# Performance work log

Measured on AMD Instinct MI355X. Metric: run time of the kernel, lower is better.

## Reference

```python
import jax, jax.numpy as jnp
import numpy as np

N = 100000      # nodes
E = 3200000     # edges (avg degree 32)
NIN = 16        # node_input_channels
ECH = 16        # edge_channels
F = 10          # node_feature_channels
OUT = 32        # output_channels
ITERS = 3


def _lin(k, fan_in, fan_out):
    kw, kb = jax.random.split(k)
    s = 1.0 / np.sqrt(fan_in)
    W = jax.random.uniform(kw, (fan_in, fan_out), jnp.float32, -s, s)
    b = jax.random.uniform(kb, (fan_out,), jnp.float32, -s, s)
    return W, b


def setup_inputs() -> dict:
    key = jax.random.key(0)
    ks = jax.random.split(key, 11)
    x = jax.random.normal(ks[0], (N, NIN), jnp.float32)
    edge_index = jax.random.randint(ks[1], (2, E), 0, N, jnp.int64)
    edge_attr = jax.random.normal(ks[2], (E, ECH), jnp.float32)
    W1, b1 = _lin(ks[3], NIN, F)
    W2, b2 = _lin(ks[4], F, F)
    W3, b3 = _lin(ks[5], F, F)
    W4, b4 = _lin(ks[6], ECH, F)
    W5, b5 = _lin(ks[7], 2 * F, OUT)
    W6, b6 = _lin(ks[8], F, F)
    W7, b7 = _lin(ks[9], F, F)
    return dict(x=x, edge_index=edge_index, edge_attr=edge_attr,
                W1=W1, b1=b1, W2=W2, b2=b2, W3=W3, b3=b3, W4=W4, b4=b4,
                W5=W5, b5=b5, W6=W6, b6=b6, W7=W7, b7=b7)


def reference(x, edge_index, edge_attr, W1, b1, W2, b2, W3, b3, W4, b4, W5, b5, W6, b6, W7, b7):
    src = edge_index[0]
    dst = edge_index[1]
    n = x.shape[0]

    # loop-invariant pieces (same math, hoisted)
    o1 = x @ W1 + b1                                   # lin1(x), [N, F]
    e = jax.nn.relu(edge_attr @ W4 + b4)               # relu(lin4(edge_attr)), [E, F]
    o3 = jax.ops.segment_sum(e, dst, num_segments=n) @ W3 + b3  # lin3(scatter_add)

    features = jnp.zeros((n, F), x.dtype)
    for _ in range(ITERS):
        # scatter_add over edges with self-loops == segment_sum + identity
        agg = jax.ops.segment_sum(features[src], dst, num_segments=n) + features
        o2 = agg @ W2 + b2
        features = jax.nn.relu(o1 + o2 + o3)

    g = features.sum(axis=0) @ W6 + b6                 # lin6(sum), [F]
    h1 = jnp.broadcast_to(g, (n, F))                   # repeat over nodes
    h2 = features @ W7 + b7                            # lin7(features)
    out = jax.nn.relu(jnp.concatenate([h1, h2], axis=1)) @ W5 + b5
    return out
```

## Files before the change

### kernel.cpp

```cpp
#include <hip/hip_runtime.h>

#define NN 100000
#define NE 3200000
#define NIN 16
#define ECH 16
#define F 10
#define FP 16
#define OC 32
#define CSB 104
#define BKSH 7
#define NBK 782
#define CH 8192
#define CAP 5120

__device__ __forceinline__ unsigned pk_bf16(float a, float b) {
    unsigned ua = __float_as_uint(a); ua = (ua + 0x7FFFu + ((ua >> 16) & 1u)) >> 16;
    unsigned ub = __float_as_uint(b); ub = (ub + 0x7FFFu + ((ub >> 16) & 1u)) >> 16;
    return ua | (ub << 16);
}
__device__ __forceinline__ float bf_lo(unsigned u) { return __uint_as_float(u << 16); }
__device__ __forceinline__ float bf_hi(unsigned u) { return __uint_as_float(u & 0xFFFF0000u); }

__global__ __launch_bounds__(256) void k_binscat(
    const int* __restrict__ src, const int* __restrict__ dst,
    int* __restrict__ cur, int2* __restrict__ pair)
{
    __shared__ int lcnt[NBK];
    __shared__ int lbb[NBK];
    int t = threadIdx.x;
    int e0 = blockIdx.x * CH;
    int e1 = e0 + CH; if (e1 > NE) e1 = NE;
    for (int k = t; k < NBK; k += 256) lcnt[k] = 0;
    __syncthreads();
    for (int e = e0 + t; e < e1; e += 256)
        atomicAdd(&lcnt[dst[e] >> BKSH], 1);
    __syncthreads();
    for (int k = t; k < NBK; k += 256) {
        int c = lcnt[k];
        lbb[k] = c ? (k * CAP + atomicAdd(&cur[k], c)) : 0;
        lcnt[k] = 0;
    }
    __syncthreads();
    for (int e = e0 + t; e < e1; e += 256) {
        int d = dst[e];
        int bk = d >> BKSH;
        int idx = atomicAdd(&lcnt[bk], 1);
        pair[lbb[bk] + idx] = make_int2(src[e], ((d & 127) << 22) | e);
    }
}

__global__ __launch_bounds__(1024) void k_bkscan(const int* __restrict__ cnt,
                                                 int* __restrict__ bkbase,
                                                 int* __restrict__ offs)
{
    __shared__ int wsum[16], wscan[16];
    int t = threadIdx.x;
    int v = (t < NBK) ? cnt[t] : 0;
    int lane = t & 63, w = t >> 6;
    int inc = v;
    for (int d = 1; d < 64; d <<= 1) { int u = __shfl_up(inc, d); if (lane >= d) inc += u; }
    if (lane == 63) wsum[w] = inc;
    __syncthreads();
    if (t < 16) {
        int u = wsum[t];
        for (int d = 1; d < 16; d <<= 1) { int x2 = __shfl_up(u, d); if (t >= d) u += x2; }
        wscan[t] = u;
    }
    __syncthreads();
    int excl = inc - v + (w > 0 ? wscan[w - 1] : 0);
    if (t < NBK) bkbase[t] = excl;
    if (t == 0) { bkbase[NBK] = NE; offs[NN] = NE; }
}

__global__ __launch_bounds__(256) void k_lsort(
    const int* __restrict__ bkbase, const int2* __restrict__ pair,
    int* __restrict__ offs, int* __restrict__ srcs, int* __restrict__ eids)
{
    __shared__ int lcnt[128];
    __shared__ int lcur[128];
    __shared__ int s0tot;
    int t = threadIdx.x;
    int b = blockIdx.x;
    int base = bkbase[b];
    int cnt = bkbase[b + 1] - base;
    const int2* tp = pair + (size_t)b * CAP;
    int n0 = b << BKSH;
    int nodes = NN - n0; if (nodes > 128) nodes = 128;

    if (t < 128) lcnt[t] = 0;
    __syncthreads();
    for (int i = t; i < cnt; i += 256)
        atomicAdd(&lcnt[((unsigned)tp[i].y) >> 22], 1);
    __syncthreads();
    if (t < 128) {
        int v = lcnt[t];
        int lane = t & 63, w = t >> 6;
        int inc = v;
        for (int d = 1; d < 64; d <<= 1) { int u = __shfl_up(inc, d); if (lane >= d) inc += u; }
        if (w == 0 && lane == 63) s0tot = inc;
        __syncthreads();
        int excl = inc - v + (w == 1 ? s0tot : 0);
        lcur[t] = base + excl;
        if (t < nodes) offs[n0 + t] = base + excl;
    } else {
        __syncthreads();
    }
    __syncthreads();
    for (int i = t; i < cnt; i += 256) {
        int2 pr = tp[i];
        int pe = pr.y;
        int pos = atomicAdd(&lcur[((unsigned)pe) >> 22], 1);
        srcs[pos] = pr.x;
        eids[pos] = pe & 0x3FFFFF;
    }
}

__global__ __launch_bounds__(256) void k_init(
    const float* __restrict__ x, const float* __restrict__ ea,
    const int* __restrict__ eids, const int* __restrict__ offs,
    const float* __restrict__ W1, const float* __restrict__ b1,
    const float* __restrict__ b2,
    const float* __restrict__ W3, const float* __restrict__ b3,
    const float* __restrict__ W4, const float* __restrict__ b4,
    float* __restrict__ base, unsigned* __restrict__ fb)
{
    __shared__ float w1[NIN*F], w3[F*F], w4[ECH*F], bb[F], b4s[F];
    int t = threadIdx.x;
    if (t < NIN*F) w1[t] = W1[t];
    if (t < F*F)   w3[t] = W3[t];
    if (t < ECH*F) w4[t] = W4[t];
    if (t < F) { bb[t] = b1[t] + b2[t] + b3[t]; b4s[t] = b4[t]; }
    __syncthreads();

    int wid = t >> 6, l = t & 63;
    int n = blockIdx.x * 4 + wid;
    bool valid = n < NN;
    int p0 = 0, p1 = 0;
    if (valid) { p0 = offs[n]; p1 = offs[n + 1]; }
    int g = l >> 2, sub = l & 3;
    int ib = sub * 4;

    float acc[F];
#pragma unroll
    for (int j = 0; j < F; ++j) acc[j] = 0.f;

    int p = p0 + g;
    for (; p + 16 < p1; p += 32) {
        int e0 = eids[p], e1 = eids[p + 16];
        float4 av0 = ((const float4*)(ea + (size_t)e0 * ECH))[sub];
        float4 av1 = ((const float4*)(ea + (size_t)e1 * ECH))[sub];
        float ev0[F], ev1[F];
#pragma unroll
        for (int j = 0; j < F; ++j) {
            float s0 = fmaf(av0.x, w4[(ib+0)*F + j], 0.f);
            s0 = fmaf(av0.y, w4[(ib+1)*F + j], s0);
            s0 = fmaf(av0.z, w4[(ib+2)*F + j], s0);
            s0 = fmaf(av0.w, w4[(ib+3)*F + j], s0);
            ev0[j] = s0;
            float s1 = fmaf(av1.x, w4[(ib+0)*F + j], 0.f);
            s1 = fmaf(av1.y, w4[(ib+1)*F + j], s1);
            s1 = fmaf(av1.z, w4[(ib+2)*F + j], s1);
            s1 = fmaf(av1.w, w4[(ib+3)*F + j], s1);
            ev1[j] = s1;
        }
#pragma unroll
        for (int j = 0; j < F; ++j) { ev0[j] += __shfl_xor(ev0[j], 1); ev1[j] += __shfl_xor(ev1[j], 1); }
#pragma unroll
        for (int j = 0; j < F; ++j) { ev0[j] += __shfl_xor(ev0[j], 2); ev1[j] += __shfl_xor(ev1[j], 2); }
#pragma unroll
        for (int j = 0; j < F; ++j)
            acc[j] += fmaxf(ev0[j] + b4s[j], 0.f) + fmaxf(ev1[j] + b4s[j], 0.f);
    }
    if (p < p1) {
        int e0 = eids[p];
        float4 av = ((const float4*)(ea + (size_t)e0 * ECH))[sub];
        float ev[F];
#pragma unroll
        for (int j = 0; j < F; ++j) {
            float s0 = fmaf(av.x, w4[(ib+0)*F + j], 0.f);
            s0 = fmaf(av.y, w4[(ib+1)*F + j], s0);
            s0 = fmaf(av.z, w4[(ib+2)*F + j], s0);
            s0 = fmaf(av.w, w4[(ib+3)*F + j], s0);
            ev[j] = s0;
        }
#pragma unroll
        for (int j = 0; j < F; ++j) ev[j] += __shfl_xor(ev[j], 1);
#pragma unroll
        for (int j = 0; j < F; ++j) ev[j] += __shfl_xor(ev[j], 2);
#pragma unroll
        for (int j = 0; j < F; ++j) acc[j] += fmaxf(ev[j] + b4s[j], 0.f);
    }
#pragma unroll
    for (int m = 4; m < 64; m <<= 1) {
#pragma unroll
        for (int j = 0; j < F; ++j) acc[j] += __shfl_xor(acc[j], m);
    }

    float fv = 0.f;
    if (valid) {
        int j = l;
        if (j < F) {
            float a = bb[j];
#pragma unroll
            for (int i = 0; i < NIN; ++i)
                a = fmaf(x[(size_t)n * NIN + i], w1[i*F + j], a);
#pragma unroll
            for (int i = 0; i < F; ++i)
                a = fmaf(acc[i], w3[i*F + j], a);
            base[(size_t)n * FP + j] = a;
            fv = fmaxf(a, 0.f);
        } else if (j < FP) {
            base[(size_t)n * FP + j] = 0.f;
        }
    }
    float partner = __shfl_xor(fv, 1);
    if (valid && l < 16 && (l & 1) == 0)
        fb[(size_t)n * 8 + (l >> 1)] = pk_bf16(fv, partner);
}

__global__ __launch_bounds__(256) void k_iter(
    const int* __restrict__ srcs, const int* __restrict__ offs,
    const uint2* __restrict__ fbO, const float* __restrict__ base,
    const float* __restrict__ W2,
    unsigned* __restrict__ fbN, float* __restrict__ featN,
    int wfb, int wf32)
{
    __shared__ float w2[F*F];
    __shared__ float sm[4][16];
    int t = threadIdx.x;
    if (t < F*F) w2[t] = W2[t];
    __syncthreads();

    int wid = t >> 6, l = t & 63;
    int n = blockIdx.x * 4 + wid;
    bool valid = n < NN;
    int p0 = 0, p1 = 0;
    if (valid) { p0 = offs[n]; p1 = offs[n + 1]; }
    int g = l >> 2, sub = l & 3;

    float4 a4 = make_float4(0.f, 0.f, 0.f, 0.f);
    int p = p0 + g;
    for (; p + 16 < p1; p += 32) {
        int s0 = srcs[p], s1 = srcs[p + 16];
        uint2 v0 = fbO[(size_t)s0 * 4 + sub];
        uint2 v1 = fbO[(size_t)s1 * 4 + sub];
        a4.x += bf_lo(v0.x) + bf_lo(v1.x);
        a4.y += bf_hi(v0.x) + bf_hi(v1.x);
        a4.z += bf_lo(v0.y) + bf_lo(v1.y);
        a4.w += bf_hi(v0.y) + bf_hi(v1.y);
    }
    if (p < p1) {
        int s0 = srcs[p];
        uint2 v0 = fbO[(size_t)s0 * 4 + sub];
        a4.x += bf_lo(v0.x); a4.y += bf_hi(v0.x);
        a4.z += bf_lo(v0.y); a4.w += bf_hi(v0.y);
    }
#pragma unroll
    for (int m = 4; m < 64; m <<= 1) {
        a4.x += __shfl_xor(a4.x, m); a4.y += __shfl_xor(a4.y, m);
        a4.z += __shfl_xor(a4.z, m); a4.w += __shfl_xor(a4.w, m);
    }
    if (valid && l < 4) {
        uint2 sv = fbO[(size_t)n * 4 + l];
        sm[wid][l*4+0] = a4.x + bf_lo(sv.x); sm[wid][l*4+1] = a4.y + bf_hi(sv.x);
        sm[wid][l*4+2] = a4.z + bf_lo(sv.y); sm[wid][l*4+3] = a4.w + bf_hi(sv.y);
    }
    __syncthreads();
    float fv = 0.f;
    if (valid && l < F) {
        float a = base[(size_t)n * FP + l];
#pragma unroll
        for (int i = 0; i < F; ++i)
            a = fmaf(sm[wid][i], w2[i*F + l], a);
        fv = fmaxf(a, 0.f);
    }
    float partner = __shfl_xor(fv, 1);
    if (valid) {
        if (wfb && l < 16 && (l & 1) == 0)
            fbN[(size_t)n * 8 + (l >> 1)] = pk_bf16(fv, partner);
        if (wf32) {
            if (l < F) featN[(size_t)n * FP + l] = fv;
            else if (l < FP) featN[(size_t)n * FP + l] = 0.f;
        }
    }
}

__global__ __launch_bounds__(256) void k_colsum(
    const float* __restrict__ feat, float* __restrict__ cpart)
{
    __shared__ float sm[4][F];
    int t = threadIdx.x;
    float v[F];
#pragma unroll
    for (int j = 0; j < F; ++j) v[j] = 0.f;
    for (int n = blockIdx.x * 256 + t; n < NN; n += CSB * 256) {
        const float4* p = (const float4*)(feat + (size_t)n * FP);
        float4 v0 = p[0], v1 = p[1], v2 = p[2];
        v[0]+=v0.x; v[1]+=v0.y; v[2]+=v0.z; v[3]+=v0.w;
        v[4]+=v1.x; v[5]+=v1.y; v[6]+=v1.z; v[7]+=v1.w;
        v[8]+=v2.x; v[9]+=v2.y;
    }
#pragma unroll
    for (int off = 32; off > 0; off >>= 1) {
#pragma unroll
        for (int j = 0; j < F; ++j) v[j] += __shfl_down(v[j], off);
    }
    int wid = t >> 6;
    if ((t & 63) == 0) {
#pragma unroll
        for (int j = 0; j < F; ++j) sm[wid][j] = v[j];
    }
    __syncthreads();
    if (t < F) {
        float s = sm[0][t] + sm[1][t] + sm[2][t] + sm[3][t];
        cpart[blockIdx.x * F + t] = s;
    }
}

__global__ void k_gsmall(
    const float* __restrict__ cpart, const float* __restrict__ W6,
    const float* __restrict__ b6, const float* __restrict__ W5,
    const float* __restrict__ b5, float* __restrict__ gpart)
{
    __shared__ float gcol[F], r1[F];
    int t = threadIdx.x;
    if (t < F) {
        float s = 0.f;
        for (int b = 0; b < CSB; ++b) s += cpart[b * F + t];
        gcol[t] = s;
    }
    __syncthreads();
    if (t < F) {
        float acc = b6[t];
        for (int i = 0; i < F; ++i) acc = fmaf(gcol[i], W6[i*F + t], acc);
        r1[t] = acc > 0.f ? acc : 0.f;
    }
    __syncthreads();
    if (t < OC) {
        float acc = b5[t];
        for (int i = 0; i < F; ++i) acc = fmaf(r1[i], W5[i*OC + t], acc);
        gpart[t] = acc;
    }
}

__global__ __launch_bounds__(256) void k_out(
    const float* __restrict__ feat, const float* __restrict__ W7,
    const float* __restrict__ b7, const float* __restrict__ W5,
    const float* __restrict__ gpart, float* __restrict__ out)
{
    __shared__ float w7[F*F], bb7[F], w5[F*OC], gp[OC];
    int t = threadIdx.x;
    if (t < F*F) w7[t] = W7[t];
    if (t < F) bb7[t] = b7[t];
    for (int i = t; i < F*OC; i += 256) w5[i] = W5[F*OC + i];
    if (t < OC) gp[t] = gpart[t];
    __syncthreads();
    int n = blockIdx.x * 256 + t;
    if (n >= NN) return;
    const float4* p = (const float4*)(feat + (size_t)n * FP);
    float4 v0 = p[0], v1 = p[1], v2 = p[2];
    float f[F] = {v0.x,v0.y,v0.z,v0.w, v1.x,v1.y,v1.z,v1.w, v2.x,v2.y};
    float h[F];
#pragma unroll
    for (int j = 0; j < F; ++j) h[j] = bb7[j];
#pragma unroll
    for (int i = 0; i < F; ++i) {
        float fi = f[i];
#pragma unroll
        for (int j = 0; j < F; ++j) h[j] = fmaf(fi, w7[i*F + j], h[j]);
    }
#pragma unroll
    for (int j = 0; j < F; ++j) h[j] = h[j] > 0.f ? h[j] : 0.f;
    float o[OC];
#pragma unroll
    for (int k = 0; k < OC; ++k) o[k] = gp[k];
#pragma unroll
    for (int j = 0; j < F; ++j) {
        float hj = h[j];
#pragma unroll
        for (int k = 0; k < OC; ++k) o[k] = fmaf(hj, w5[j*OC + k], o[k]);
    }
    float4* po = (float4*)(out + (size_t)n * OC);
#pragma unroll
    for (int k = 0; k < 8; ++k)
        po[k] = make_float4(o[4*k], o[4*k+1], o[4*k+2], o[4*k+3]);
}

extern "C" void kernel_launch(void* const* d_in, const int* in_sizes, int n_in,
                              void* d_out, int out_size, void* d_ws, size_t ws_size,
                              hipStream_t stream)
{
    const float* x   = (const float*)d_in[0];
    const int*   ei  = (const int*)d_in[1];
    const float* ea  = (const float*)d_in[2];
    const float* W1  = (const float*)d_in[3];
    const float* b1  = (const float*)d_in[4];
    const float* W2  = (const float*)d_in[5];
    const float* b2  = (const float*)d_in[6];
    const float* W3  = (const float*)d_in[7];
    const float* b3  = (const float*)d_in[8];
    const float* W4  = (const float*)d_in[9];
    const float* b4  = (const float*)d_in[10];
    const float* W5  = (const float*)d_in[11];
    const float* b5  = (const float*)d_in[12];
    const float* W6  = (const float*)d_in[13];
    const float* b6  = (const float*)d_in[14];
    const float* W7  = (const float*)d_in[15];
    const float* b7  = (const float*)d_in[16];

    const int* src = ei;
    const int* dst = ei + NE;

    char* w = (char*)d_ws;
    int2* pair   = (int2*)w;                   w += (size_t)NBK * CAP * 8;
    int* srcs    = (int*)w;                    w += (size_t)NE * 4;
    int* eids    = (int*)w;                    w += (size_t)NE * 4;
    float* base  = (float*)w;                  w += (size_t)NN * FP * 4;
    float* featA = (float*)w;                  w += (size_t)NN * FP * 4;
    unsigned* fbA = (unsigned*)w;              w += (size_t)NN * 32;
    unsigned* fbB = (unsigned*)w;              w += (size_t)NN * 32;
    int* offs    = (int*)w;                    w += (size_t)(NN + 16) * 4;
    int* cur     = (int*)w;                    w += (size_t)NBK * 4;
    int* bkbase  = (int*)w;                    w += (size_t)(NBK + 16) * 4;
    float* cpart = (float*)w;                  w += (size_t)CSB * F * 4;
    float* gpart = (float*)w;                  w += 32 * 4;

    const int NB = (NN + 255) / 256;
    const int WB = (NN + 3) / 4;
    const int SB = (NE + CH - 1) / CH;

    hipMemsetAsync(cur, 0, (size_t)NBK * 4, stream);

    k_binscat<<<SB, 256, 0, stream>>>(src, dst, cur, pair);
    k_bkscan <<<1, 1024, 0, stream>>>(cur, bkbase, offs);
    k_lsort  <<<NBK, 256, 0, stream>>>(bkbase, pair, offs, srcs, eids);

    k_init   <<<WB, 256, 0, stream>>>(x, ea, eids, offs, W1, b1, b2, W3, b3,
                                      W4, b4, base, fbA);

    k_iter   <<<WB, 256, 0, stream>>>(srcs, offs, (const uint2*)fbA, base, W2,
                                      fbB, (float*)nullptr, 1, 0);
    k_iter   <<<WB, 256, 0, stream>>>(srcs, offs, (const uint2*)fbB, base, W2,
                                      (unsigned*)nullptr, featA, 0, 1);

    k_colsum <<<CSB, 256, 0, stream>>>(featA, cpart);
    k_gsmall <<<1, 64, 0, stream>>>(cpart, W6, b6, W5, b5, gpart);
    k_out    <<<NB, 256, 0, stream>>>(featA, W7, b7, W5, gpart, (float*)d_out);
}
```

Baseline: 434.9 us.

## Keep final features in bf16 and cache dst values in registers during binning

The last propagation iteration now writes only the packed bf16 feature buffer instead of a padded fp32 copy, and the column-sum and output kernels read and unpack bf16. This cuts the memory traffic of the final iteration and of the two readers, at the cost of extra rounding in the final features. The binning kernel also loads dst values once into a 32-entry register array and reuses them in the scatter pass, so dst is not read twice, at the cost of more registers per thread.

Result: faster. 425.9 us (-2.1%).

```diff
diff --git a/kernel.cpp b/kernel.cpp
--- a/kernel.cpp
+++ b/kernel.cpp
@@ -11,6 +11,7 @@
 #define BKSH 7
 #define NBK 782
 #define CH 8192
+#define NIT 32
 #define CAP 5120
 
 __device__ __forceinline__ unsigned pk_bf16(float a, float b) {
@@ -32,8 +33,13 @@
     int e1 = e0 + CH; if (e1 > NE) e1 = NE;
     for (int k = t; k < NBK; k += 256) lcnt[k] = 0;
     __syncthreads();
-    for (int e = e0 + t; e < e1; e += 256)
-        atomicAdd(&lcnt[dst[e] >> BKSH], 1);
+    int dv[NIT];
+#pragma unroll
+    for (int it = 0; it < NIT; ++it) {
+        int e = e0 + t + it * 256;
+        dv[it] = (e < e1) ? dst[e] : -1;
+        if (dv[it] >= 0) atomicAdd(&lcnt[dv[it] >> BKSH], 1);
+    }
     __syncthreads();
     for (int k = t; k < NBK; k += 256) {
         int c = lcnt[k];
@@ -41,11 +47,15 @@
         lcnt[k] = 0;
     }
     __syncthreads();
-    for (int e = e0 + t; e < e1; e += 256) {
-        int d = dst[e];
-        int bk = d >> BKSH;
-        int idx = atomicAdd(&lcnt[bk], 1);
-        pair[lbb[bk] + idx] = make_int2(src[e], ((d & 127) << 22) | e);
+#pragma unroll
+    for (int it = 0; it < NIT; ++it) {
+        int e = e0 + t + it * 256;
+        int d = dv[it];
+        if (d >= 0) {
+            int bk = d >> BKSH;
+            int idx = atomicAdd(&lcnt[bk], 1);
+            pair[lbb[bk] + idx] = make_int2(src[e], ((d & 127) << 22) | e);
+        }
     }
 }
 
@@ -221,9 +231,7 @@
 __global__ __launch_bounds__(256) void k_iter(
     const int* __restrict__ srcs, const int* __restrict__ offs,
     const uint2* __restrict__ fbO, const float* __restrict__ base,
-    const float* __restrict__ W2,
-    unsigned* __restrict__ fbN, float* __restrict__ featN,
-    int wfb, int wf32)
+    const float* __restrict__ W2, unsigned* __restrict__ fbN)
 {
     __shared__ float w2[F*F];
     __shared__ float sm[4][16];
@@ -275,18 +283,12 @@
         fv = fmaxf(a, 0.f);
     }
     float partner = __shfl_xor(fv, 1);
-    if (valid) {
-        if (wfb && l < 16 && (l & 1) == 0)
-            fbN[(size_t)n * 8 + (l >> 1)] = pk_bf16(fv, partner);
-        if (wf32) {
-            if (l < F) featN[(size_t)n * FP + l] = fv;
-            else if (l < FP) featN[(size_t)n * FP + l] = 0.f;
-        }
-    }
+    if (valid && l < 16 && (l & 1) == 0)
+        fbN[(size_t)n * 8 + (l >> 1)] = pk_bf16(fv, partner);
 }
 
 __global__ __launch_bounds__(256) void k_colsum(
-    const float* __restrict__ feat, float* __restrict__ cpart)
+    const unsigned* __restrict__ fb, float* __restrict__ cpart)
 {
     __shared__ float sm[4][F];
     int t = threadIdx.x;
@@ -294,11 +296,14 @@
 #pragma unroll
     for (int j = 0; j < F; ++j) v[j] = 0.f;
     for (int n = blockIdx.x * 256 + t; n < NN; n += CSB * 256) {
-        const float4* p = (const float4*)(feat + (size_t)n * FP);
-        float4 v0 = p[0], v1 = p[1], v2 = p[2];
-        v[0]+=v0.x; v[1]+=v0.y; v[2]+=v0.z; v[3]+=v0.w;
-        v[4]+=v1.x; v[5]+=v1.y; v[6]+=v1.z; v[7]+=v1.w;
-        v[8]+=v2.x; v[9]+=v2.y;
+        const uint4* p = (const uint4*)(fb + (size_t)n * 8);
+        uint4 a = p[0];
+        unsigned b = fb[(size_t)n * 8 + 4];
+        v[0]+=bf_lo(a.x); v[1]+=bf_hi(a.x);
+        v[2]+=bf_lo(a.y); v[3]+=bf_hi(a.y);
+        v[4]+=bf_lo(a.z); v[5]+=bf_hi(a.z);
+        v[6]+=bf_lo(a.w); v[7]+=bf_hi(a.w);
+        v[8]+=bf_lo(b);   v[9]+=bf_hi(b);
     }
 #pragma unroll
     for (int off = 32; off > 0; off >>= 1) {
@@ -344,7 +349,7 @@
 }
 
 __global__ __launch_bounds__(256) void k_out(
-    const float* __restrict__ feat, const float* __restrict__ W7,
+    const unsigned* __restrict__ fb, const float* __restrict__ W7,
     const float* __restrict__ b7, const float* __restrict__ W5,
     const float* __restrict__ gpart, float* __restrict__ out)
 {
@@ -357,9 +362,12 @@
     __syncthreads();
     int n = blockIdx.x * 256 + t;
     if (n >= NN) return;
-    const float4* p = (const float4*)(feat + (size_t)n * FP);
-    float4 v0 = p[0], v1 = p[1], v2 = p[2];
-    float f[F] = {v0.x,v0.y,v0.z,v0.w, v1.x,v1.y,v1.z,v1.w, v2.x,v2.y};
+    const uint4* p = (const uint4*)(fb + (size_t)n * 8);
+    uint4 a = p[0];
+    unsigned b = fb[(size_t)n * 8 + 4];
+    float f[F] = {bf_lo(a.x), bf_hi(a.x), bf_lo(a.y), bf_hi(a.y),
+                  bf_lo(a.z), bf_hi(a.z), bf_lo(a.w), bf_hi(a.w),
+                  bf_lo(b),   bf_hi(b)};
     float h[F];
 #pragma unroll
     for (int j = 0; j < F; ++j) h[j] = bb7[j];
@@ -416,7 +424,6 @@
     int* srcs    = (int*)w;                    w += (size_t)NE * 4;
     int* eids    = (int*)w;                    w += (size_t)NE * 4;
     float* base  = (float*)w;                  w += (size_t)NN * FP * 4;
-    float* featA = (float*)w;                  w += (size_t)NN * FP * 4;
     unsigned* fbA = (unsigned*)w;              w += (size_t)NN * 32;
     unsigned* fbB = (unsigned*)w;              w += (size_t)NN * 32;
     int* offs    = (int*)w;                    w += (size_t)(NN + 16) * 4;
@@ -438,12 +445,10 @@
     k_init   <<<WB, 256, 0, stream>>>(x, ea, eids, offs, W1, b1, b2, W3, b3,
                                       W4, b4, base, fbA);
 
-    k_iter   <<<WB, 256, 0, stream>>>(srcs, offs, (const uint2*)fbA, base, W2,
-                                      fbB, (float*)nullptr, 1, 0);
-    k_iter   <<<WB, 256, 0, stream>>>(srcs, offs, (const uint2*)fbB, base, W2,
-                                      (unsigned*)nullptr, featA, 0, 1);
-
-    k_colsum <<<CSB, 256, 0, stream>>>(featA, cpart);
+    k_iter   <<<WB, 256, 0, stream>>>(srcs, offs, (const uint2*)fbA, base, W2, fbB);
+    k_iter   <<<WB, 256, 0, stream>>>(srcs, offs, (const uint2*)fbB, base, W2, fbA);
+
+    k_colsum <<<CSB, 256, 0, stream>>>(fbA, cpart);
     k_gsmall <<<1, 64, 0, stream>>>(cpart, W6, b6, W5, b5, gpart);
-    k_out    <<<NB, 256, 0, stream>>>(featA, W7, b7, W5, gpart, (float*)d_out);
-}
+    k_out    <<<NB, 256, 0, stream>>>(fbA, W7, b7, W5, gpart, (float*)d_out);
+}
```
